# Kernel tuning notes

Hardware: AMD Instinct MI355X
Metric: run time of the kernel (lower is better)

The kernel has to match this reference:

```python
import jax, jax.numpy as jnp
import numpy as np
from functools import partial

INPUT_DIM = 256
HIDDEN = 512
NUM_LAYERS = 2

def _linp(key, fan_in, shape):
    # torch nn.Linear/Conv default init: U(-1/sqrt(fan_in), 1/sqrt(fan_in))
    bound = 1.0 / np.sqrt(fan_in)
    return jax.random.uniform(key, shape, jnp.float32, -bound, bound)

def setup_inputs() -> dict:
    key = jax.random.key(0)
    ks = iter(jax.random.split(key, 64))
    d = {}
    d["x"] = jax.random.normal(next(ks), (32, 16, 1, 64, 64), jnp.float32)
    # encoder convs (OIHW)
    d["conv1_w"] = _linp(next(ks), 1 * 9, (16, 1, 3, 3));   d["conv1_b"] = _linp(next(ks), 1 * 9, (16,))
    d["conv2_w"] = _linp(next(ks), 16 * 9, (32, 16, 3, 3)); d["conv2_b"] = _linp(next(ks), 16 * 9, (32,))
    d["conv3_w"] = _linp(next(ks), 32 * 9, (INPUT_DIM, 32, 3, 3)); d["conv3_b"] = _linp(next(ks), 32 * 9, (INPUT_DIM,))
    # LSTM cells: per layer 4 gate linears (forget, input, cell, output), in = input+hidden
    for j in range(NUM_LAYERS):
        fan = (INPUT_DIM if j == 0 else HIDDEN) + HIDDEN
        for g in ("f", "i", "g", "o"):
            d[f"W{g}{j}"] = _linp(next(ks), fan, (fan, HIDDEN))
            d[f"b{g}{j}"] = _linp(next(ks), fan, (HIDDEN,))
    # classifier
    d["cw1"] = _linp(next(ks), HIDDEN, (HIDDEN, 128)); d["cb1"] = _linp(next(ks), HIDDEN, (128,))
    d["cw2"] = _linp(next(ks), 128, (128, 64));        d["cb2"] = _linp(next(ks), 128, (64,))
    d["cw3"] = _linp(next(ks), 64, (64, 6));           d["cb3"] = _linp(next(ks), 64, (6,))
    return d

def _conv(x, w, b):
    y = jax.lax.conv_general_dilated(x, w, (1, 1), "SAME",
                                     dimension_numbers=("NCHW", "OIHW", "NCHW"))
    return y + b[None, :, None, None]

def _maxpool2(x):
    return jax.lax.reduce_window(x, -jnp.inf, jax.lax.max,
                                 (1, 1, 2, 2), (1, 1, 2, 2), "VALID")

def reference(x, conv1_w, conv1_b, conv2_w, conv2_b, conv3_w, conv3_b,
              Wf0, bf0, Wi0, bi0, Wg0, bg0, Wo0, bo0,
              Wf1, bf1, Wi1, bi1, Wg1, bg1, Wo1, bo1,
              cw1, cb1, cw2, cb2, cw3, cb3):
    B, T, C, H, W = x.shape
    xf = x.reshape(B * T, C, H, W)
    h = _maxpool2(jax.nn.relu(_conv(xf, conv1_w, conv1_b)))
    h = _maxpool2(jax.nn.relu(_conv(h, conv2_w, conv2_b)))
    h = jax.nn.relu(_conv(h, conv3_w, conv3_b))
    emb = h.mean(axis=(2, 3)).reshape(B, T, -1)  # AdaptiveAvgPool2d((1,1)); dropout = identity (eval)

    layers = [(Wf0, bf0, Wi0, bi0, Wg0, bg0, Wo0, bo0),
              (Wf1, bf1, Wi1, bi1, Wg1, bg1, Wo1, bo1)]

    def step(carry, x_t):
        hs, cs = carry
        inp = x_t
        new_h, new_c = [], []
        for j, (Wf, bf, Wi, bi, Wg, bg, Wo, bo) in enumerate(layers):
            comb = jnp.concatenate([inp, hs[j]], axis=1)  # [B, in+H]
            f_t = jax.nn.sigmoid(comb @ Wf + bf)
            i_t = jax.nn.sigmoid(comb @ Wi + bi)
            g_t = jnp.tanh(comb @ Wg + bg)
            o_t = jax.nn.sigmoid(comb @ Wo + bo)
            c_n = f_t * cs[j] + i_t * g_t
            h_n = o_t * jnp.tanh(c_n)
            new_h.append(h_n); new_c.append(c_n)
            inp = h_n
        return (tuple(new_h), tuple(new_c)), None

    h0 = tuple(jnp.zeros((B, HIDDEN), x.dtype) for _ in range(NUM_LAYERS))
    c0 = tuple(jnp.zeros((B, HIDDEN), x.dtype) for _ in range(NUM_LAYERS))
    (hs, _), _ = jax.lax.scan(step, (h0, c0), jnp.swapaxes(emb, 0, 1))
    last = hs[-1]  # [B, HIDDEN], last timestep top-layer h (dropout = identity)

    y = jax.nn.relu(last @ cw1 + cb1)
    y = jax.nn.relu(y @ cw2 + cb2)
    return y @ cw3 + cb3  # [B, 6]
```

## Files before the change

kernel.cpp:

```cpp
#include <hip/hip_runtime.h>
#include <math.h>

__global__ void k_conv1(const float* __restrict__ x, const float* __restrict__ w,
                        const float* __restrict__ bias, float* __restrict__ out) {
  int idx = blockIdx.x * 256 + threadIdx.x;
  int ox = idx & 31, oy = (idx >> 5) & 31, oc = (idx >> 10) & 15, n = idx >> 14;
  const float* im = x + n * 4096;
  float wv[9];
#pragma unroll
  for (int i = 0; i < 9; ++i) wv[i] = w[oc * 9 + i];
  float bs = bias[oc];
  float m = 0.f;
#pragma unroll
  for (int dy = 0; dy < 2; ++dy)
#pragma unroll
    for (int dx = 0; dx < 2; ++dx) {
      int cy = oy * 2 + dy, cx = ox * 2 + dx;
      float s = bs;
#pragma unroll
      for (int ky = 0; ky < 3; ++ky) {
        int yy = cy + ky - 1;
        if (yy < 0 || yy >= 64) continue;
#pragma unroll
        for (int kx = 0; kx < 3; ++kx) {
          int xx = cx + kx - 1;
          if (xx < 0 || xx >= 64) continue;
          s += im[yy * 64 + xx] * wv[ky * 3 + kx];
        }
      }
      m = fmaxf(m, fmaxf(s, 0.f));
    }
  out[idx] = m;
}

__global__ void k_prep_w(const float* __restrict__ w2, float* __restrict__ w2t,
                         const float* __restrict__ w3, float* __restrict__ w3t) {
  int id = blockIdx.x * 256 + threadIdx.x;
  if (id < 73728) {
    int ct = id >> 8, oc = id & 255;
    int c = ct / 9, tap = ct - 9 * c;
    w3t[id] = w3[(oc * 32 + c) * 9 + tap];
  }
  if (id < 4608) {
    int ct = id >> 5, oc = id & 31;
    int c = ct / 9, tap = ct - 9 * c;
    w2t[id] = w2[(oc * 16 + c) * 9 + tap];
  }
}

__global__ __launch_bounds__(256) void k_conv2(
    const float* __restrict__ a1, const float* __restrict__ w2t,
    const float* __restrict__ bias, float* __restrict__ a2) {
  __shared__ __align__(16) float ins[8 * 1024];
  int n = blockIdx.x, ocg = blockIdx.y;
  int tid = threadIdx.x;
  int py = tid >> 4, px = tid & 15;
  int y0 = 2 * py - 1, x0 = 2 * px - 1;
  float acc[16][4] = {};
  const float* wb = w2t + ocg * 16;
  for (int ph = 0; ph < 2; ++ph) {
    __syncthreads();
    const float4* src = (const float4*)(a1 + n * 16384 + ph * 8192);
    for (int i = tid; i < 2048; i += 256) ((float4*)ins)[i] = src[i];
    __syncthreads();
    for (int c = 0; c < 8; ++c) {
      float wv[4][4];
#pragma unroll
      for (int r = 0; r < 4; ++r) {
        int y = y0 + r;
        bool vy = (y >= 0) && (y < 32);
        int yc = vy ? y : 0;
#pragma unroll
        for (int cc = 0; cc < 4; ++cc) {
          int xx = x0 + cc;
          bool vx = (xx >= 0) && (xx < 32);
          int xc = vx ? xx : 0;
          float t = ins[c * 1024 + yc * 32 + xc];
          wv[r][cc] = (vy && vx) ? t : 0.f;
        }
      }
      int ch = ph * 8 + c;
#pragma unroll
      for (int ky = 0; ky < 3; ++ky)
#pragma unroll
        for (int kx = 0; kx < 3; ++kx) {
          const float* w16 = wb + (ch * 9 + ky * 3 + kx) * 32;
#pragma unroll
          for (int i = 0; i < 4; ++i) {
            float vv = wv[(i >> 1) + ky][(i & 1) + kx];
#pragma unroll
            for (int j = 0; j < 16; ++j) acc[j][i] += vv * w16[j];
          }
        }
    }
  }
  const float* bp = bias + ocg * 16;
  float4 o[4];
#pragma unroll
  for (int j = 0; j < 16; ++j) {
    float m = fmaxf(fmaxf(acc[j][0], acc[j][1]), fmaxf(acc[j][2], acc[j][3]));
    ((float*)o)[j] = fmaxf(m + bp[j], 0.f);
  }
  float4* dst = (float4*)(a2 + (size_t)(n * 256 + tid) * 32 + ocg * 16);
#pragma unroll
  for (int q = 0; q < 4; ++q) dst[q] = o[q];
}

__global__ __launch_bounds__(256) void k_conv3(
    const float* __restrict__ a2, const float* __restrict__ w3t,
    const float* __restrict__ bias, float* __restrict__ comb0) {
  __shared__ __align__(16) float ins[324 * 20];
  int n = blockIdx.x, ocb = blockIdx.y;
  int tid = threadIdx.x;
  for (int i = tid; i < 1620; i += 256) ((float4*)ins)[i] = float4{0.f, 0.f, 0.f, 0.f};
  int wvid = __builtin_amdgcn_readfirstlane(tid >> 6);
  int lane = tid & 63;
  int tr = lane >> 4, tc = lane & 15;
  float acc[4][8] = {};
  const float* wbase = w3t + ocb * 32 + wvid * 8;
  const float4* src = (const float4*)(a2 + (size_t)n * 8192);
  for (int hf = 0; hf < 2; ++hf) {
    __syncthreads();
    for (int i = tid; i < 1024; i += 256) {
      int px = i >> 2, cg = i & 3;
      int p = ((px >> 4) + 1) * 18 + (px & 15) + 1;
      ((float4*)ins)[p * 5 + cg] = src[px * 8 + hf * 4 + cg];
    }
    __syncthreads();
    for (int cg = 0; cg < 4; ++cg) {
      float4 v[6][3];
#pragma unroll
      for (int dr = 0; dr < 6; ++dr)
#pragma unroll
        for (int dc = 0; dc < 3; ++dc)
          v[dr][dc] = ((const float4*)ins)[((4 * tr + dr) * 18 + tc + dc) * 5 + cg];
#pragma unroll
      for (int ky = 0; ky < 3; ++ky)
#pragma unroll
        for (int kx = 0; kx < 3; ++kx)
#pragma unroll
          for (int c = 0; c < 4; ++c) {
            const float* w8 = wbase + (((hf * 4 + cg) * 4 + c) * 9 + ky * 3 + kx) * 256;
#pragma unroll
            for (int i = 0; i < 4; ++i) {
              float vv = ((const float*)&v[i + ky][kx])[c];
#pragma unroll
              for (int j = 0; j < 8; ++j) acc[i][j] += vv * w8[j];
            }
          }
    }
  }
  const float* bp = bias + ocb * 32 + wvid * 8;
  int bb = n >> 4, tt = n & 15;
#pragma unroll
  for (int j = 0; j < 8; ++j) {
    float bj = bp[j];
    float s = 0.f;
#pragma unroll
    for (int i = 0; i < 4; ++i) s += fmaxf(acc[i][j] + bj, 0.f);
#pragma unroll
    for (int off = 32; off; off >>= 1) s += __shfl_down(s, off, 64);
    if (lane == 0) {
      int oc = ocb * 32 + wvid * 8 + j;
      comb0[(size_t)(tt * 768 + oc) * 32 + bb] = s * (1.f / 256.f);
    }
  }
}

__global__ void k_pack(const float* __restrict__ Wf, const float* __restrict__ Wi,
                       const float* __restrict__ Wg, const float* __restrict__ Wo,
                       float* __restrict__ p, int fan) {
  __shared__ float t[4][32][33];
  int k0 = blockIdx.x * 32, h0 = blockIdx.y * 32;
  int tx = threadIdx.x & 31, ty = threadIdx.x >> 5;
  const float* Ws[4] = {Wf, Wi, Wg, Wo};
#pragma unroll
  for (int g = 0; g < 4; ++g)
    for (int r = 0; r < 32; r += 8)
      t[g][ty + r][tx] = Ws[g][(size_t)(k0 + ty + r) * 512 + h0 + tx];
  __syncthreads();
  for (int r = 0; r < 32; r += 8) {
    int hh = ty + r;
    float4 v = {t[0][tx][hh], t[1][tx][hh], t[2][tx][hh], t[3][tx][hh]};
    ((float4*)p)[(size_t)(h0 + hh) * fan + k0 + tx] = v;
  }
}

struct Coop2Args {
  float* comb0; float* comb1;
  const float* p0; const float* p1;
  const float* b00; const float* b01; const float* b02; const float* b03;
  const float* b10; const float* b11; const float* b12; const float* b13;
  int* bar;
};

#define COOP2_LDS_BYTES (23040 * 4)

template <int FAN>
__device__ __forceinline__ void coop_step(
    int hbase, int tid, const float* __restrict__ comb,
    const float* __restrict__ wl,
    float* __restrict__ houtA, float* __restrict__ houtB,
    float bfv, float biv, float bgv, float bov,
    float& creg, float* __restrict__ gsum, float* __restrict__ pre) {
  constexpr int CH = FAN / 32;
  const int hs = tid >> 8, kc = (tid >> 3) & 31, bq = tid & 7;
  const float4* w4 = (const float4*)wl + (size_t)hs * FAN + kc * CH;
  const float4* a4 = (const float4*)comb;
  const int rot = kc & 7;
  float4 af{0,0,0,0}, ai{0,0,0,0}, ag{0,0,0,0}, ao{0,0,0,0};
#pragma unroll
  for (int kk = 0; kk < CH; ++kk) {
    int idx = kk + rot; if (idx >= CH) idx -= CH;
    float4 w = w4[idx];
    float4 a = a4[(size_t)(kc * CH + idx) * 8 + bq];
    af.x += w.x*a.x; af.y += w.x*a.y; af.z += w.x*a.z; af.w += w.x*a.w;
    ai.x += w.y*a.x; ai.y += w.y*a.y; ai.z += w.y*a.z; ai.w += w.y*a.w;
    ag.x += w.z*a.x; ag.y += w.z*a.y; ag.z += w.z*a.z; ag.w += w.z*a.w;
    ao.x += w.w*a.x; ao.y += w.w*a.y; ao.z += w.w*a.z; ao.w += w.w*a.w;
  }
  __syncthreads();
  {
    const float* accs[4] = {(const float*)&af, (const float*)&ai,
                            (const float*)&ag, (const float*)&ao};
#pragma unroll
    for (int g = 0; g < 4; ++g)
#pragma unroll
      for (int j = 0; j < 4; ++j)
        gsum[((hs * 4 + g) * 32 + 4 * bq + j) * 33 + kc] = accs[g][j];
  }
  __syncthreads();
  if (tid < 256) {
    int hs2 = tid >> 7, g = (tid >> 5) & 3, b = tid & 31;
    int base = ((hs2 * 4 + g) * 32 + b) * 33;
    float s = 0.f;
#pragma unroll
    for (int q = 0; q < 32; ++q) s += gsum[base + q];
    pre[(hs2 * 4 + g) * 32 + b] = s;
  }
  __syncthreads();
  if (tid < 64) {
    int hs2 = tid >> 5, b = tid & 31;
    float fp = pre[(hs2 * 4 + 0) * 32 + b] + bfv;
    float ip = pre[(hs2 * 4 + 1) * 32 + b] + biv;
    float gp = pre[(hs2 * 4 + 2) * 32 + b] + bgv;
    float op = pre[(hs2 * 4 + 3) * 32 + b] + bov;
    float ft = 1.f / (1.f + expf(-fp));
    float it_ = 1.f / (1.f + expf(-ip));
    float gt = tanhf(gp);
    float ot = 1.f / (1.f + expf(-op));
    float cn = ft * creg + it_ * gt;
    creg = cn;
    float hn = ot * tanhf(cn);
    int hh = hbase + hs2;
    __hip_atomic_store(&houtA[hh * 32 + b], hn, __ATOMIC_RELAXED,
                       __HIP_MEMORY_SCOPE_AGENT);
    if (houtB != houtA)
      __hip_atomic_store(&houtB[hh * 32 + b], hn, __ATOMIC_RELAXED,
                         __HIP_MEMORY_SCOPE_AGENT);
  }
}

__global__ __launch_bounds__(512) void k_lstm_coop2(Coop2Args A) {
  extern __shared__ float smem[];
  float* wl0 = smem;
  float* wl1 = smem + 6144;
  float* gsum = smem + 14336;
  float* pre = smem + 22784;
  const int tid = threadIdx.x;
  const int hbase = blockIdx.x * 2;
  for (int i = tid; i < 1536; i += 512) {
    int hs = i / 768, k = i - hs * 768;
    ((float4*)wl0)[hs * 768 + k] =
        ((const float4*)A.p0)[(size_t)(hbase + hs) * 768 + k];
  }
  for (int i = tid; i < 2048; i += 512) {
    int hs = i >> 10, k = i & 1023;
    ((float4*)wl1)[hs * 1024 + k] =
        ((const float4*)A.p1)[(size_t)(hbase + hs) * 1024 + k];
  }
  float bf0 = 0, bi0 = 0, bg0 = 0, bo0 = 0;
  float bf1 = 0, bi1 = 0, bg1 = 0, bo1 = 0;
  if (tid < 64) {
    int hh = hbase + (tid >> 5);
    bf0 = A.b00[hh]; bi0 = A.b01[hh]; bg0 = A.b02[hh]; bo0 = A.b03[hh];
    bf1 = A.b10[hh]; bi1 = A.b11[hh]; bg1 = A.b12[hh]; bo1 = A.b13[hh];
  }
  __syncthreads();
  float c0reg = 0.f, c1reg = 0.f;
  const int C0 = 768 * 32, C1 = 1024 * 32;
  for (int it = 0; it <= 16; ++it) {
    if (it < 16)
      coop_step<768>(hbase, tid, A.comb0 + (size_t)it * C0, wl0,
                     A.comb0 + (size_t)(it + 1) * C0 + 256 * 32,
                     A.comb1 + (size_t)it * C1,
                     bf0, bi0, bg0, bo0, c0reg, gsum, pre);
    if (it >= 1)
      coop_step<1024>(hbase, tid, A.comb1 + (size_t)(it - 1) * C1, wl1,
                      A.comb1 + (size_t)it * C1 + 512 * 32,
                      A.comb1 + (size_t)it * C1 + 512 * 32,
                      bf1, bi1, bg1, bo1, c1reg, gsum, pre);
    if (it < 16) {
      __syncthreads();
      if (tid == 0) {
        __hip_atomic_fetch_add(A.bar, 1, __ATOMIC_RELEASE,
                               __HIP_MEMORY_SCOPE_AGENT);
        const int target = 256 * (it + 1);
        while (__hip_atomic_load(A.bar, __ATOMIC_RELAXED,
                                 __HIP_MEMORY_SCOPE_AGENT) < target)
          __builtin_amdgcn_s_sleep(8);
        __builtin_amdgcn_fence(__ATOMIC_ACQUIRE, "agent");
      }
      __syncthreads();
    }
  }
}

struct SArgs {
  const float* comb; const float* pw;
  float* houtA; float* houtB; float* cT;
  const float* bf; const float* bi; const float* bg; const float* bo;
};

template <int FAN>
__device__ __forceinline__ void lstm_sbody(int h, int tid, const SArgs& A,
                                           float* __restrict__ gsum) {
  constexpr int CH = FAN / 8;
  const int wv = __builtin_amdgcn_readfirstlane(tid >> 6);
  const int lane = tid & 63;
  const int ks = lane >> 5, b = lane & 31;
  const int kb = wv * CH;
  const float4* pw4 = (const float4*)A.pw + (size_t)h * FAN + kb;
  const float* ac = A.comb + (size_t)kb * 32 + lane;
  float a0 = 0.f, a1 = 0.f, a2 = 0.f, a3 = 0.f;
#pragma unroll 8
  for (int kk = 0; kk < CH; kk += 2) {
    float4 w0 = pw4[kk];
    float4 w1 = pw4[kk + 1];
    float av = ac[kk * 32];
    a0 += av * (ks ? w1.x : w0.x);
    a1 += av * (ks ? w1.y : w0.y);
    a2 += av * (ks ? w1.z : w0.z);
    a3 += av * (ks ? w1.w : w0.w);
  }
  a0 += __shfl_xor(a0, 32);
  a1 += __shfl_xor(a1, 32);
  a2 += __shfl_xor(a2, 32);
  a3 += __shfl_xor(a3, 32);
  if (lane < 32) {
    gsum[(wv * 4 + 0) * 33 + b] = a0;
    gsum[(wv * 4 + 1) * 33 + b] = a1;
    gsum[(wv * 4 + 2) * 33 + b] = a2;
    gsum[(wv * 4 + 3) * 33 + b] = a3;
  }
  __syncthreads();
  if (tid < 32) {
    float fp = A.bf[h], ip = A.bi[h], gp = A.bg[h], op = A.bo[h];
#pragma unroll
    for (int q = 0; q < 8; ++q) {
      fp += gsum[(q * 4 + 0) * 33 + tid];
      ip += gsum[(q * 4 + 1) * 33 + tid];
      gp += gsum[(q * 4 + 2) * 33 + tid];
      op += gsum[(q * 4 + 3) * 33 + tid];
    }
    float ft = 1.f / (1.f + expf(-fp));
    float it_ = 1.f / (1.f + expf(-ip));
    float gt = tanhf(gp);
    float ot = 1.f / (1.f + expf(-op));
    float cn = ft * A.cT[h * 32 + tid] + it_ * gt;
    A.cT[h * 32 + tid] = cn;
    float hn = ot * tanhf(cn);
    A.houtA[h * 32 + tid] = hn;
    A.houtB[h * 32 + tid] = hn;
  }
}

__global__ __launch_bounds__(512) void k_lstm_s0(SArgs a) {
  __shared__ float gsum[32 * 33];
  lstm_sbody<768>(blockIdx.x, threadIdx.x, a, gsum);
}
__global__ __launch_bounds__(512) void k_lstm_s1(SArgs a) {
  __shared__ float gsum[32 * 33];
  lstm_sbody<1024>(blockIdx.x, threadIdx.x, a, gsum);
}
__global__ __launch_bounds__(512) void k_lstm_spair(SArgs a0, SArgs a1) {
  __shared__ float gsum[32 * 33];
  if (blockIdx.x < 512)
    lstm_sbody<768>(blockIdx.x, threadIdx.x, a0, gsum);
  else
    lstm_sbody<1024>(blockIdx.x - 512, threadIdx.x, a1, gsum);
}

__global__ void k_cls(const float* __restrict__ h1T, const float* __restrict__ cw1,
                      const float* __restrict__ cb1, const float* __restrict__ cw2,
                      const float* __restrict__ cb2, const float* __restrict__ cw3,
                      const float* __restrict__ cb3, float* __restrict__ out) {
  __shared__ float hv[512];
  __shared__ float y1[128];
  __shared__ float y2[64];
  int b = blockIdx.x, tid = threadIdx.x;
  for (int i = tid; i < 512; i += 128) hv[i] = h1T[i * 32 + b];
  __syncthreads();
  float s = cb1[tid];
  for (int k = 0; k < 512; ++k) s += hv[k] * cw1[k * 128 + tid];
  y1[tid] = fmaxf(s, 0.f);
  __syncthreads();
  if (tid < 64) {
    float s2 = cb2[tid];
    for (int k = 0; k < 128; ++k) s2 += y1[k] * cw2[k * 64 + tid];
    y2[tid] = fmaxf(s2, 0.f);
  }
  __syncthreads();
  if (tid < 6) {
    float s3 = cb3[tid];
    for (int k = 0; k < 64; ++k) s3 += y2[k] * cw3[k * 6 + tid];
    out[b * 6 + tid] = s3;
  }
}

extern "C" void kernel_launch(void* const* d_in, const int* in_sizes, int n_in,
                              void* d_out, int out_size, void* d_ws, size_t ws_size,
                              hipStream_t stream) {
  const float* x  = (const float*)d_in[0];
  const float* w1 = (const float*)d_in[1];
  const float* b1 = (const float*)d_in[2];
  const float* w2 = (const float*)d_in[3];
  const float* b2 = (const float*)d_in[4];
  const float* w3 = (const float*)d_in[5];
  const float* b3 = (const float*)d_in[6];
  const float* cw1 = (const float*)d_in[23];
  const float* cb1 = (const float*)d_in[24];
  const float* cw2 = (const float*)d_in[25];
  const float* cb2 = (const float*)d_in[26];
  const float* cw3 = (const float*)d_in[27];
  const float* cb3 = (const float*)d_in[28];

  float* ws = (float*)d_ws;
  float* a1    = ws;
  float* p0    = ws;
  float* p1    = ws + 1572864;
  float* comb0 = ws + 3670016;
  float* comb1 = ws + 4087808;
  float* c0    = ws + 4644864;
  float* c1    = ws + 4661248;
  int*   bar   = (int*)(ws + 4677632);
  float* a2    = ws + 8388608;
  float* w2t   = ws + 12582912;
  float* w3t   = ws + 12587520;
  const int C0 = 768 * 32, C1 = 1024 * 32;

  k_prep_w<<<288, 256, 0, stream>>>(w2, w2t, w3, w3t);
  k_conv1<<<32768, 256, 0, stream>>>(x, w1, b1, a1);
  k_conv2<<<dim3(512, 2), 256, 0, stream>>>(a1, w2t, b2, a2);

  hipMemsetAsync(comb0 + 256 * 32, 0, (size_t)512 * 32 * 4, stream);
  hipMemsetAsync(comb1 + 512 * 32, 0, (size_t)512 * 32 * 4, stream);
  hipMemsetAsync(c0, 0, (size_t)2 * 512 * 32 * 4, stream);
  hipMemsetAsync(bar, 0, sizeof(int), stream);

  k_conv3<<<dim3(512, 8), 256, 0, stream>>>(a2, w3t, b3, comb0);

  k_pack<<<dim3(24, 16), 256, 0, stream>>>(
      (const float*)d_in[7], (const float*)d_in[9],
      (const float*)d_in[11], (const float*)d_in[13], p0, 768);
  k_pack<<<dim3(32, 16), 256, 0, stream>>>(
      (const float*)d_in[15], (const float*)d_in[17],
      (const float*)d_in[19], (const float*)d_in[21], p1, 1024);

  Coop2Args ca;
  ca.comb0 = comb0; ca.comb1 = comb1;
  ca.p0 = p0; ca.p1 = p1;
  ca.b00 = (const float*)d_in[8];  ca.b01 = (const float*)d_in[10];
  ca.b02 = (const float*)d_in[12]; ca.b03 = (const float*)d_in[14];
  ca.b10 = (const float*)d_in[16]; ca.b11 = (const float*)d_in[18];
  ca.b12 = (const float*)d_in[20]; ca.b13 = (const float*)d_in[22];
  ca.bar = bar;
  void* kargs[] = {&ca};
  hipError_t cerr = hipLaunchCooperativeKernel(
      (void*)k_lstm_coop2, dim3(256), dim3(512), kargs, COOP2_LDS_BYTES, stream);

  if (cerr != hipSuccess) {
    auto L0 = [&](int t) {
      SArgs a;
      a.comb = comb0 + (size_t)t * C0;
      a.pw = p0;
      a.houtA = comb0 + (size_t)(t + 1) * C0 + 256 * 32;
      a.houtB = comb1 + (size_t)t * C1;
      a.cT = c0;
      a.bf = (const float*)d_in[8];  a.bi = (const float*)d_in[10];
      a.bg = (const float*)d_in[12]; a.bo = (const float*)d_in[14];
      return a;
    };
    auto L1 = [&](int t) {
      SArgs a;
      a.comb = comb1 + (size_t)t * C1;
      a.pw = p1;
      a.houtA = comb1 + (size_t)(t + 1) * C1 + 512 * 32;
      a.houtB = a.houtA;
      a.cT = c1;
      a.bf = (const float*)d_in[16]; a.bi = (const float*)d_in[18];
      a.bg = (const float*)d_in[20]; a.bo = (const float*)d_in[22];
      return a;
    };
    k_lstm_s0<<<512, 512, 0, stream>>>(L0(0));
    for (int p = 0; p < 15; ++p)
      k_lstm_spair<<<1024, 512, 0, stream>>>(L0(p + 1), L1(p));
    k_lstm_s1<<<512, 512, 0, stream>>>(L1(15));
  }

  k_cls<<<32, 128, 0, stream>>>(comb1 + (size_t)16 * C1 + 512 * 32,
                                cw1, cb1, cw2, cb2, cw3, cb3, (float*)d_out);
}
```

Measured before the change: 617.4 us.

## Fuse both LSTM layer steps into one interleaved pass per wavefront step

Replaces the two sequential per-layer coop_step calls with a single fused loop that accumulates layer-0 and layer-1 gate dot products in the same unrolled loop. Separate LDS reduction buffers let both layers share one set of barriers, the reduction and the activation phase, roughly halving the __syncthreads count per timestep. Each layer's cell state is spread across different threads. The cost is more registers (eight float4 accumulators) and a larger LDS footprint.

```diff
diff --git a/kernel.cpp b/kernel.cpp
--- a/kernel.cpp
+++ b/kernel.cpp
@@ -194,83 +194,20 @@
   int* bar;
 };
 
-#define COOP2_LDS_BYTES (23040 * 4)
-
-template <int FAN>
-__device__ __forceinline__ void coop_step(
-    int hbase, int tid, const float* __restrict__ comb,
-    const float* __restrict__ wl,
-    float* __restrict__ houtA, float* __restrict__ houtB,
-    float bfv, float biv, float bgv, float bov,
-    float& creg, float* __restrict__ gsum, float* __restrict__ pre) {
-  constexpr int CH = FAN / 32;
-  const int hs = tid >> 8, kc = (tid >> 3) & 31, bq = tid & 7;
-  const float4* w4 = (const float4*)wl + (size_t)hs * FAN + kc * CH;
-  const float4* a4 = (const float4*)comb;
-  const int rot = kc & 7;
-  float4 af{0,0,0,0}, ai{0,0,0,0}, ag{0,0,0,0}, ao{0,0,0,0};
-#pragma unroll
-  for (int kk = 0; kk < CH; ++kk) {
-    int idx = kk + rot; if (idx >= CH) idx -= CH;
-    float4 w = w4[idx];
-    float4 a = a4[(size_t)(kc * CH + idx) * 8 + bq];
-    af.x += w.x*a.x; af.y += w.x*a.y; af.z += w.x*a.z; af.w += w.x*a.w;
-    ai.x += w.y*a.x; ai.y += w.y*a.y; ai.z += w.y*a.z; ai.w += w.y*a.w;
-    ag.x += w.z*a.x; ag.y += w.z*a.y; ag.z += w.z*a.z; ag.w += w.z*a.w;
-    ao.x += w.w*a.x; ao.y += w.w*a.y; ao.z += w.w*a.z; ao.w += w.w*a.w;
-  }
-  __syncthreads();
-  {
-    const float* accs[4] = {(const float*)&af, (const float*)&ai,
-                            (const float*)&ag, (const float*)&ao};
-#pragma unroll
-    for (int g = 0; g < 4; ++g)
-#pragma unroll
-      for (int j = 0; j < 4; ++j)
-        gsum[((hs * 4 + g) * 32 + 4 * bq + j) * 33 + kc] = accs[g][j];
-  }
-  __syncthreads();
-  if (tid < 256) {
-    int hs2 = tid >> 7, g = (tid >> 5) & 3, b = tid & 31;
-    int base = ((hs2 * 4 + g) * 32 + b) * 33;
-    float s = 0.f;
-#pragma unroll
-    for (int q = 0; q < 32; ++q) s += gsum[base + q];
-    pre[(hs2 * 4 + g) * 32 + b] = s;
-  }
-  __syncthreads();
-  if (tid < 64) {
-    int hs2 = tid >> 5, b = tid & 31;
-    float fp = pre[(hs2 * 4 + 0) * 32 + b] + bfv;
-    float ip = pre[(hs2 * 4 + 1) * 32 + b] + biv;
-    float gp = pre[(hs2 * 4 + 2) * 32 + b] + bgv;
-    float op = pre[(hs2 * 4 + 3) * 32 + b] + bov;
-    float ft = 1.f / (1.f + expf(-fp));
-    float it_ = 1.f / (1.f + expf(-ip));
-    float gt = tanhf(gp);
-    float ot = 1.f / (1.f + expf(-op));
-    float cn = ft * creg + it_ * gt;
-    creg = cn;
-    float hn = ot * tanhf(cn);
-    int hh = hbase + hs2;
-    __hip_atomic_store(&houtA[hh * 32 + b], hn, __ATOMIC_RELAXED,
-                       __HIP_MEMORY_SCOPE_AGENT);
-    if (houtB != houtA)
-      __hip_atomic_store(&houtB[hh * 32 + b], hn, __ATOMIC_RELAXED,
-                         __HIP_MEMORY_SCOPE_AGENT);
-  }
-}
+#define COOP2_LDS_BYTES (31744 * 4)
 
 __global__ __launch_bounds__(512) void k_lstm_coop2(Coop2Args A) {
   extern __shared__ float smem[];
   float* wl0 = smem;
   float* wl1 = smem + 6144;
-  float* gsum = smem + 14336;
-  float* pre = smem + 22784;
+  float* gsum0 = smem + 14336;
+  float* gsum1 = smem + 22784;
+  float* pre = smem + 31232;
   const int tid = threadIdx.x;
   const int hbase = blockIdx.x * 2;
+  const int C0 = 768 * 32, C1 = 1024 * 32;
   for (int i = tid; i < 1536; i += 512) {
-    int hs = i / 768, k = i - hs * 768;
+    int hs = (i >= 768), k = i - hs * 768;
     ((float4*)wl0)[hs * 768 + k] =
         ((const float4*)A.p0)[(size_t)(hbase + hs) * 768 + k];
   }
@@ -279,27 +216,110 @@
     ((float4*)wl1)[hs * 1024 + k] =
         ((const float4*)A.p1)[(size_t)(hbase + hs) * 1024 + k];
   }
-  float bf0 = 0, bi0 = 0, bg0 = 0, bo0 = 0;
-  float bf1 = 0, bi1 = 0, bg1 = 0, bo1 = 0;
+  float bf = 0, bi = 0, bg = 0, bo = 0, creg = 0.f;
   if (tid < 64) {
     int hh = hbase + (tid >> 5);
-    bf0 = A.b00[hh]; bi0 = A.b01[hh]; bg0 = A.b02[hh]; bo0 = A.b03[hh];
-    bf1 = A.b10[hh]; bi1 = A.b11[hh]; bg1 = A.b12[hh]; bo1 = A.b13[hh];
+    bf = A.b00[hh]; bi = A.b01[hh]; bg = A.b02[hh]; bo = A.b03[hh];
+  } else if (tid < 128) {
+    int hh = hbase + ((tid >> 5) & 1);
+    bf = A.b10[hh]; bi = A.b11[hh]; bg = A.b12[hh]; bo = A.b13[hh];
   }
   __syncthreads();
-  float c0reg = 0.f, c1reg = 0.f;
-  const int C0 = 768 * 32, C1 = 1024 * 32;
+
+  const int hs = tid >> 8, kc = (tid >> 3) & 31, bq = tid & 7;
+  const int rot = kc & 7;
+  const float4* w40 = (const float4*)wl0 + (size_t)hs * 768 + kc * 24;
+  const float4* w41 = (const float4*)wl1 + (size_t)hs * 1024 + kc * 32;
+
   for (int it = 0; it <= 16; ++it) {
-    if (it < 16)
-      coop_step<768>(hbase, tid, A.comb0 + (size_t)it * C0, wl0,
-                     A.comb0 + (size_t)(it + 1) * C0 + 256 * 32,
-                     A.comb1 + (size_t)it * C1,
-                     bf0, bi0, bg0, bo0, c0reg, gsum, pre);
-    if (it >= 1)
-      coop_step<1024>(hbase, tid, A.comb1 + (size_t)(it - 1) * C1, wl1,
-                      A.comb1 + (size_t)it * C1 + 512 * 32,
-                      A.comb1 + (size_t)it * C1 + 512 * 32,
-                      bf1, bi1, bg1, bo1, c1reg, gsum, pre);
+    const bool l0act = (it < 16), l1act = (it >= 1);
+    const float4* a40 = (const float4*)(A.comb0 + (size_t)it * C0);
+    const float4* a41 = (const float4*)(A.comb1 + (size_t)(it - 1) * C1);
+    float4 f0{0,0,0,0}, i0{0,0,0,0}, g0{0,0,0,0}, o0{0,0,0,0};
+    float4 f1{0,0,0,0}, i1{0,0,0,0}, g1{0,0,0,0}, o1{0,0,0,0};
+#pragma unroll
+    for (int kk = 0; kk < 32; ++kk) {
+      if (l1act) {
+        int idx = kk + rot; if (idx >= 32) idx -= 32;
+        float4 w = w41[idx];
+        float4 a = a41[(size_t)(kc * 32 + idx) * 8 + bq];
+        f1.x += w.x*a.x; f1.y += w.x*a.y; f1.z += w.x*a.z; f1.w += w.x*a.w;
+        i1.x += w.y*a.x; i1.y += w.y*a.y; i1.z += w.y*a.z; i1.w += w.y*a.w;
+        g1.x += w.z*a.x; g1.y += w.z*a.y; g1.z += w.z*a.z; g1.w += w.z*a.w;
+        o1.x += w.w*a.x; o1.y += w.w*a.y; o1.z += w.w*a.z; o1.w += w.w*a.w;
+      }
+      if (l0act && kk < 24) {
+        int idx = kk + rot; if (idx >= 24) idx -= 24;
+        float4 w = w40[idx];
+        float4 a = a40[(size_t)(kc * 24 + idx) * 8 + bq];
+        f0.x += w.x*a.x; f0.y += w.x*a.y; f0.z += w.x*a.z; f0.w += w.x*a.w;
+        i0.x += w.y*a.x; i0.y += w.y*a.y; i0.z += w.y*a.z; i0.w += w.y*a.w;
+        g0.x += w.z*a.x; g0.y += w.z*a.y; g0.z += w.z*a.z; g0.w += w.z*a.w;
+        o0.x += w.w*a.x; o0.y += w.w*a.y; o0.z += w.w*a.z; o0.w += w.w*a.w;
+      }
+    }
+    __syncthreads();
+    if (l0act) {
+      const float* accs[4] = {(const float*)&f0, (const float*)&i0,
+                              (const float*)&g0, (const float*)&o0};
+#pragma unroll
+      for (int g = 0; g < 4; ++g)
+#pragma unroll
+        for (int j = 0; j < 4; ++j)
+          gsum0[((hs * 4 + g) * 32 + 4 * bq + j) * 33 + kc] = accs[g][j];
+    }
+    if (l1act) {
+      const float* accs[4] = {(const float*)&f1, (const float*)&i1,
+                              (const float*)&g1, (const float*)&o1};
+#pragma unroll
+      for (int g = 0; g < 4; ++g)
+#pragma unroll
+        for (int j = 0; j < 4; ++j)
+          gsum1[((hs * 4 + g) * 32 + 4 * bq + j) * 33 + kc] = accs[g][j];
+    }
+    __syncthreads();
+    {
+      int l = tid >> 8, idx = tid & 255;
+      int hs2 = idx >> 7, g = (idx >> 5) & 3, b = idx & 31;
+      const float* gs = l ? gsum1 : gsum0;
+      int base = ((hs2 * 4 + g) * 32 + b) * 33;
+      float s = 0.f;
+#pragma unroll
+      for (int q = 0; q < 32; ++q) s += gs[base + q];
+      pre[l * 256 + (hs2 * 4 + g) * 32 + b] = s;
+    }
+    __syncthreads();
+    if (tid < 128) {
+      int l = tid >> 6, hs2 = (tid >> 5) & 1, b = tid & 31;
+      bool active = l ? l1act : l0act;
+      if (active) {
+        const float* pr = pre + l * 256;
+        float fp = pr[(hs2 * 4 + 0) * 32 + b] + bf;
+        float ip = pr[(hs2 * 4 + 1) * 32 + b] + bi;
+        float gp = pr[(hs2 * 4 + 2) * 32 + b] + bg;
+        float op = pr[(hs2 * 4 + 3) * 32 + b] + bo;
+        float ft = 1.f / (1.f + expf(-fp));
+        float it_ = 1.f / (1.f + expf(-ip));
+        float gt = tanhf(gp);
+        float ot = 1.f / (1.f + expf(-op));
+        float cn = ft * creg + it_ * gt;
+        creg = cn;
+        float hn = ot * tanhf(cn);
+        int hh = hbase + hs2;
+        if (l == 0) {
+          float* hA = A.comb0 + (size_t)(it + 1) * C0 + 256 * 32;
+          float* hB = A.comb1 + (size_t)it * C1;
+          __hip_atomic_store(&hA[hh * 32 + b], hn, __ATOMIC_RELAXED,
+                             __HIP_MEMORY_SCOPE_AGENT);
+          __hip_atomic_store(&hB[hh * 32 + b], hn, __ATOMIC_RELAXED,
+                             __HIP_MEMORY_SCOPE_AGENT);
+        } else {
+          float* hA = A.comb1 + (size_t)it * C1 + 512 * 32;
+          __hip_atomic_store(&hA[hh * 32 + b], hn, __ATOMIC_RELAXED,
+                             __HIP_MEMORY_SCOPE_AGENT);
+        }
+      }
+    }
     if (it < 16) {
       __syncthreads();
       if (tid == 0) {
```

Result: slower. 814.4 us (+31.9%).
